# Kernel optimization log

Measured on AMD Instinct MI355X. Metric: run time of the kernel, lower is better.

## Reference

```python
import jax, jax.numpy as jnp
import numpy as np

QB = 127.0  # 2**(8-1) - 1


def ternary_dequant(w):
    # absmean ternary quantization, then dequantize by scale
    scale = jnp.mean(jnp.abs(w))
    w_t = jnp.clip(jnp.round(w / (scale + 1e-8)), -1.0, 1.0)
    w_t = jnp.where(scale == 0.0, jnp.zeros_like(w), w_t)
    return w_t * scale


def activation_quantize(x):
    # per-row (last-dim) absmax int8 fake-quant
    scale = jnp.max(jnp.abs(x), axis=-1, keepdims=True) / QB
    scale = jnp.maximum(scale, 1e-8)
    return jnp.clip(jnp.round(x / scale), -QB, QB) * scale


def setup_inputs() -> dict:
    key = jax.random.key(0)
    kx, kw = jax.random.split(key)
    x = jax.random.normal(kx, (2, 4096, 4096), dtype=jnp.float32)
    # kaiming_uniform-ish init scale; exact init distribution is irrelevant to the math
    bound = 1.0 / np.sqrt(4096)
    weight = jax.random.uniform(kw, (4096, 4096), dtype=jnp.float32,
                                minval=-bound, maxval=bound)
    return {"x": x, "weight": weight}


def reference(x, weight):
    w_q = ternary_dequant(weight)        # [out, in]
    x_q = activation_quantize(x)         # [b, s, in]
    return jnp.einsum('bsi,oi->bso', x_q, w_q)
```

## Files before the change

### kernel.cpp

```cpp
#include <hip/hip_runtime.h>
#include <stdint.h>
#include <stddef.h>


#define K_DIM 4096
#define M_DIM 8192
#define N_DIM 4096

typedef int v4i __attribute__((ext_vector_type(4)));

__device__ __forceinline__ void async_copy16(void* lds, const void* g) {
  __builtin_amdgcn_global_load_lds(
      (const __attribute__((address_space(1))) unsigned int*)g,
      (__attribute__((address_space(3))) unsigned int*)lds,
      16, 0, 0);
}

__global__ void k_wsum(const float* __restrict__ w, double* __restrict__ partials) {
  const float4* w4 = (const float4*)w;
  int tid = blockIdx.x * 256 + threadIdx.x;
  double s = 0.0;
  for (int i = tid; i < 4194304; i += 262144) {
    float4 v = w4[i];
    s += (double)fabsf(v.x) + (double)fabsf(v.y) +
         (double)fabsf(v.z) + (double)fabsf(v.w);
  }
  for (int off = 32; off > 0; off >>= 1) s += __shfl_down(s, off);
  __shared__ double lsum[4];
  int lane = threadIdx.x & 63, wid = threadIdx.x >> 6;
  if (lane == 0) lsum[wid] = s;
  __syncthreads();
  if (threadIdx.x == 0)
    partials[blockIdx.x] = lsum[0] + lsum[1] + lsum[2] + lsum[3];
}

__global__ void k_wscale(const double* __restrict__ partials, float* __restrict__ wscale) {
  double s = 0.0;
  for (int i = threadIdx.x; i < 1024; i += 256) s += partials[i];
  for (int off = 32; off > 0; off >>= 1) s += __shfl_down(s, off);
  __shared__ double lsum[4];
  int lane = threadIdx.x & 63, wid = threadIdx.x >> 6;
  if (lane == 0) lsum[wid] = s;
  __syncthreads();
  if (threadIdx.x == 0) {
    double tot = lsum[0] + lsum[1] + lsum[2] + lsum[3];
    *wscale = (float)(tot / 16777216.0);
  }
}

__global__ void k_wq(const float* __restrict__ w, const float* __restrict__ wscale,
                     char* __restrict__ qw) {
  float d = *wscale + 1e-8f;
  const float4* w4 = (const float4*)w;
  int* q4 = (int*)qw;
  int tid = blockIdx.x * 256 + threadIdx.x;
  for (int i = tid; i < 4194304; i += 524288) {
    float4 v = w4[i];
    int a = (int)fmaxf(fminf(rintf(v.x / d), 1.f), -1.f);
    int b = (int)fmaxf(fminf(rintf(v.y / d), 1.f), -1.f);
    int c = (int)fmaxf(fminf(rintf(v.z / d), 1.f), -1.f);
    int e = (int)fmaxf(fminf(rintf(v.w / d), 1.f), -1.f);
    q4[i] = (a & 255) | ((b & 255) << 8) | ((c & 255) << 16) | ((e & 255) << 24);
  }
}

__global__ void k_xq(const float* __restrict__ x, char* __restrict__ qx,
                     float* __restrict__ sx) {
  int row = blockIdx.x;
  const float4* xr = (const float4*)(x + (size_t)row * K_DIM);
  float4 v[4];
  float m = 0.f;
#pragma unroll
  for (int c = 0; c < 4; c++) {
    v[c] = xr[threadIdx.x + c * 256];
    m = fmaxf(m, fmaxf(fmaxf(fabsf(v[c].x), fabsf(v[c].y)),
                       fmaxf(fabsf(v[c].z), fabsf(v[c].w))));
  }
  for (int off = 32; off > 0; off >>= 1) m = fmaxf(m, __shfl_down(m, off));
  __shared__ float lm[4];
  __shared__ float bscale;
  int lane = threadIdx.x & 63, wid = threadIdx.x >> 6;
  if (lane == 0) lm[wid] = m;
  __syncthreads();
  if (threadIdx.x == 0) {
    float mm = fmaxf(fmaxf(lm[0], lm[1]), fmaxf(lm[2], lm[3]));
    float sc = fmaxf(mm / 127.0f, 1e-8f);
    bscale = sc;
    sx[row] = sc;
  }
  __syncthreads();
  float sc = bscale;
  int* q4 = (int*)(qx + (size_t)row * K_DIM);
#pragma unroll
  for (int c = 0; c < 4; c++) {
    int a = (int)fmaxf(fminf(rintf(v[c].x / sc), 127.f), -127.f);
    int b = (int)fmaxf(fminf(rintf(v[c].y / sc), 127.f), -127.f);
    int cc = (int)fmaxf(fminf(rintf(v[c].z / sc), 127.f), -127.f);
    int e = (int)fmaxf(fminf(rintf(v[c].w / sc), 127.f), -127.f);
    q4[threadIdx.x + c * 256] = (a & 255) | ((b & 255) << 8) | ((cc & 255) << 16) | ((e & 255) << 24);
  }
}

__global__ __launch_bounds__(512, 2) void k_gemm(const char* __restrict__ qx,
                       const char* __restrict__ qw,
                       const float* __restrict__ sx,
                       const float* __restrict__ wscale,
                       float* __restrict__ out) {
  __shared__ char lds[4][32768];

  const int tid = threadIdx.x;
  const int lane = tid & 63;
  const int wave = tid >> 6;
  const int wr = wave >> 2;
  const int wc = wave & 3;

  const int wg = (blockIdx.x & 7) * 64 + (blockIdx.x >> 3);
  const int bm = wg >> 4;
  const int bn = wg & 15;
  const int rowBase = bm * 256;
  const int colBase = bn * 256;

  const int rl = tid >> 2;
  const int kswz = (((tid & 3) ^ ((rl >> 1) & 3)) << 4);
  const char* gA0 = qx + (size_t)(rowBase + rl) * K_DIM + kswz;
  const char* gA1 = gA0 + (size_t)128 * K_DIM;
  const char* gB0 = qw + (size_t)(colBase + rl) * K_DIM + kswz;
  const char* gB1 = gB0 + (size_t)128 * K_DIM;
  const int dOff = wave << 10;

  const int sR = ((lane & 15) >> 1) & 3;
  const int kro = (((lane >> 4) ^ sR) << 4);
  const int aOff = ((wr << 7) + (lane & 15)) * 64 + kro;
  const int bOff = 16384 + ((wc << 6) + (lane & 15)) * 64 + kro;

  v4i acc[8][4] = {};

  auto STAGE = [&](int t) {
    char* b = &lds[t & 3][0];
    const size_t ko = (size_t)t << 6;
    async_copy16(b + dOff,         gA0 + ko);
    async_copy16(b + 8192 + dOff,  gA1 + ko);
    async_copy16(b + 16384 + dOff, gB0 + ko);
    async_copy16(b + 24576 + dOff, gB1 + ko);
  };

  auto COMPUTE = [&](int t) {
    const char* b = &lds[t & 3][0];
    v4i bf[4];
#pragma unroll
    for (int n = 0; n < 4; ++n)
      bf[n] = *(const v4i*)(b + bOff + n * 1024);
    __builtin_amdgcn_s_setprio(1);
#pragma unroll
    for (int m = 0; m < 8; ++m) {
      v4i af = *(const v4i*)(b + aOff + m * 1024);
#pragma unroll
      for (int n = 0; n < 4; ++n)
        acc[m][n] = __builtin_amdgcn_mfma_i32_16x16x64_i8(af, bf[n], acc[m][n], 0, 0, 0);
    }
    __builtin_amdgcn_s_setprio(0);
  };

  STAGE(0); STAGE(1); STAGE(2);

  for (int t = 0; t < 61; ++t) {
    asm volatile("s_waitcnt vmcnt(8)" ::: "memory");
    __builtin_amdgcn_s_barrier();
    STAGE(t + 3);
    COMPUTE(t);
  }
  asm volatile("s_waitcnt vmcnt(8)" ::: "memory");
  __builtin_amdgcn_s_barrier();
  COMPUTE(61);
  asm volatile("s_waitcnt vmcnt(4)" ::: "memory");
  __builtin_amdgcn_s_barrier();
  COMPUTE(62);
  asm volatile("s_waitcnt vmcnt(0)" ::: "memory");
  __builtin_amdgcn_s_barrier();
  COMPUTE(63);

  const float swv = *wscale;
  const int col0 = colBase + (wc << 6) + (lane & 15);
  const int row0 = rowBase + (wr << 7) + ((lane >> 4) << 2);
#pragma unroll
  for (int m = 0; m < 8; ++m) {
#pragma unroll
    for (int r = 0; r < 4; ++r) {
      const int row = row0 + m * 16 + r;
      const float s = sx[row] * swv;
#pragma unroll
      for (int n = 0; n < 4; ++n)
        out[(size_t)row * N_DIM + col0 + n * 16] = (float)acc[m][n][r] * s;
    }
  }
}

extern "C" void kernel_launch(void* const* d_in, const int* in_sizes, int n_in,
                              void* d_out, int out_size, void* d_ws, size_t ws_size,
                              hipStream_t stream) {
  const float* x = (const float*)d_in[0];
  const float* w = (const float*)d_in[1];
  float* out = (float*)d_out;
  char* ws = (char*)d_ws;

  double* partials = (double*)ws;
  float* wscale    = (float*)(ws + 8192);
  float* sx        = (float*)(ws + 8448);
  char*  qw        = ws + 41472;
  char*  qx        = ws + 41472 + 16777216;

  k_wsum  <<<1024, 256, 0, stream>>>(w, partials);
  k_wscale<<<   1, 256, 0, stream>>>(partials, wscale);
  k_wq    <<<2048, 256, 0, stream>>>(w, wscale, qw);
  k_xq    <<<8192, 256, 0, stream>>>(x, qx, sx);
  k_gemm  <<<32 * 16, 512, 0, stream>>>(qx, qw, sx, wscale, out);
}
```

Measured before the change: 394.6 us.

## Split GEMM k-step into four quadrant phases interleaving loads, MFMA and barriers

Restructures the int8 GEMM main loop so each k-tile runs as four quadrant sub-phases. Each phase loads a 4x2 set of A/B fragments from LDS, issues one of the four async global-to-LDS copies for a future stage, synchronises with barriers, and runs 8 MFMAs. The goal is to interleave LDS reads, global loads and matrix-core work more finely, ping-pong style across waves. The cost is eight extra workgroup barriers per k-step and A fragments re-read from LDS twice, either of which may cut throughput.

```diff
diff --git a/kernel.cpp b/kernel.cpp
--- a/kernel.cpp
+++ b/kernel.cpp
@@ -135,49 +135,84 @@
 
   v4i acc[8][4] = {};
 
-  auto STAGE = [&](int t) {
+  auto STAGE1 = [&](int t, int q) {
     char* b = &lds[t & 3][0];
     const size_t ko = (size_t)t << 6;
-    async_copy16(b + dOff,         gA0 + ko);
-    async_copy16(b + 8192 + dOff,  gA1 + ko);
-    async_copy16(b + 16384 + dOff, gB0 + ko);
-    async_copy16(b + 24576 + dOff, gB1 + ko);
+    if (q == 0)      async_copy16(b + dOff,         gA0 + ko);
+    else if (q == 1) async_copy16(b + 8192 + dOff,  gA1 + ko);
+    else if (q == 2) async_copy16(b + 16384 + dOff, gB0 + ko);
+    else             async_copy16(b + 24576 + dOff, gB1 + ko);
   };
 
-  auto COMPUTE = [&](int t) {
-    const char* b = &lds[t & 3][0];
-    v4i bf[4];
-#pragma unroll
-    for (int n = 0; n < 4; ++n)
-      bf[n] = *(const v4i*)(b + bOff + n * 1024);
-    __builtin_amdgcn_s_setprio(1);
-#pragma unroll
-    for (int m = 0; m < 8; ++m) {
-      v4i af = *(const v4i*)(b + aOff + m * 1024);
-#pragma unroll
-      for (int n = 0; n < 4; ++n)
-        acc[m][n] = __builtin_amdgcn_mfma_i32_16x16x64_i8(af, bf[n], acc[m][n], 0, 0, 0);
-    }
-    __builtin_amdgcn_s_setprio(0);
-  };
-
-  STAGE(0); STAGE(1); STAGE(2);
+#pragma unroll
+  for (int q = 0; q < 4; ++q) STAGE1(0, q);
+#pragma unroll
+  for (int q = 0; q < 4; ++q) STAGE1(1, q);
+#pragma unroll
+  for (int q = 0; q < 4; ++q) STAGE1(2, q);
 
   for (int t = 0; t < 61; ++t) {
     asm volatile("s_waitcnt vmcnt(8)" ::: "memory");
     __builtin_amdgcn_s_barrier();
-    STAGE(t + 3);
-    COMPUTE(t);
-  }
-  asm volatile("s_waitcnt vmcnt(8)" ::: "memory");
-  __builtin_amdgcn_s_barrier();
-  COMPUTE(61);
-  asm volatile("s_waitcnt vmcnt(4)" ::: "memory");
-  __builtin_amdgcn_s_barrier();
-  COMPUTE(62);
-  asm volatile("s_waitcnt vmcnt(0)" ::: "memory");
-  __builtin_amdgcn_s_barrier();
-  COMPUTE(63);
+    const char* b = &lds[t & 3][0];
+#pragma unroll
+    for (int q = 0; q < 4; ++q) {
+      const int mh = q >> 1, nh = q & 1;
+      v4i af[4], bf[2];
+#pragma unroll
+      for (int j = 0; j < 4; ++j)
+        af[j] = *(const v4i*)(b + aOff + (mh * 4 + j) * 1024);
+#pragma unroll
+      for (int i = 0; i < 2; ++i)
+        bf[i] = *(const v4i*)(b + bOff + (nh * 2 + i) * 1024);
+      STAGE1(t + 3, q);
+      asm volatile("" ::: "memory");
+      __builtin_amdgcn_s_barrier();
+      asm volatile("s_waitcnt lgkmcnt(0)" ::: "memory");
+      __builtin_amdgcn_s_setprio(1);
+#pragma unroll
+      for (int j = 0; j < 4; ++j)
+#pragma unroll
+        for (int i = 0; i < 2; ++i)
+          acc[mh * 4 + j][nh * 2 + i] = __builtin_amdgcn_mfma_i32_16x16x64_i8(
+              af[j], bf[i], acc[mh * 4 + j][nh * 2 + i], 0, 0, 0);
+      __builtin_amdgcn_s_setprio(0);
+      __builtin_amdgcn_s_barrier();
+    }
+  }
+
+#pragma unroll
+  for (int e = 0; e < 3; ++e) {
+    const int t = 61 + e;
+    if (e == 0)      asm volatile("s_waitcnt vmcnt(8)" ::: "memory");
+    else if (e == 1) asm volatile("s_waitcnt vmcnt(4)" ::: "memory");
+    else             asm volatile("s_waitcnt vmcnt(0)" ::: "memory");
+    __builtin_amdgcn_s_barrier();
+    const char* b = &lds[t & 3][0];
+#pragma unroll
+    for (int q = 0; q < 4; ++q) {
+      const int mh = q >> 1, nh = q & 1;
+      v4i af[4], bf[2];
+#pragma unroll
+      for (int j = 0; j < 4; ++j)
+        af[j] = *(const v4i*)(b + aOff + (mh * 4 + j) * 1024);
+#pragma unroll
+      for (int i = 0; i < 2; ++i)
+        bf[i] = *(const v4i*)(b + bOff + (nh * 2 + i) * 1024);
+      asm volatile("" ::: "memory");
+      __builtin_amdgcn_s_barrier();
+      asm volatile("s_waitcnt lgkmcnt(0)" ::: "memory");
+      __builtin_amdgcn_s_setprio(1);
+#pragma unroll
+      for (int j = 0; j < 4; ++j)
+#pragma unroll
+        for (int i = 0; i < 2; ++i)
+          acc[mh * 4 + j][nh * 2 + i] = __builtin_amdgcn_mfma_i32_16x16x64_i8(
+              af[j], bf[i], acc[mh * 4 + j][nh * 2 + i], 0, 0, 0);
+      __builtin_amdgcn_s_setprio(0);
+      __builtin_amdgcn_s_barrier();
+    }
+  }
 
   const float swv = *wscale;
   const int col0 = colBase + (wc << 6) + (lane & 15);
```

New measurement: 413.2 us. 1.05x slower.

## Double-buffer LDS fragment reads in registers across k-iterations of int8 GEMM

Applied to the files above, without the earlier changes.

The GEMM main loop now prefetches the next k-tile's B fragments and first half of A fragments from LDS into a second register set while the current tile's MFMAs run, ping-ponging between two register buffers. The loop is unrolled by two with explicit prologue and epilogue, and the global-load wait is tightened so the next tile is resident before it is read. The aim is to hide LDS read latency behind MFMA work. In exchange it raises register pressure under the 512x2 launch bounds, which risks spills or lower occupancy, and it shortens the effective global prefetch distance.

```diff
diff --git a/kernel.cpp b/kernel.cpp
--- a/kernel.cpp
+++ b/kernel.cpp
@@ -144,40 +144,78 @@
     async_copy16(b + 24576 + dOff, gB1 + ko);
   };
 
-  auto COMPUTE = [&](int t) {
-    const char* b = &lds[t & 3][0];
-    v4i bf[4];
-#pragma unroll
-    for (int n = 0; n < 4; ++n)
-      bf[n] = *(const v4i*)(b + bOff + n * 1024);
-    __builtin_amdgcn_s_setprio(1);
-#pragma unroll
-    for (int m = 0; m < 8; ++m) {
-      v4i af = *(const v4i*)(b + aOff + m * 1024);
-#pragma unroll
-      for (int n = 0; n < 4; ++n)
-        acc[m][n] = __builtin_amdgcn_mfma_i32_16x16x64_i8(af, bf[n], acc[m][n], 0, 0, 0);
-    }
-    __builtin_amdgcn_s_setprio(0);
-  };
+  v4i afA[4], bfA[4], afB[4], bfB[4];
+
+#define PRE_READ(T, AF, BF)                                                  \
+  {                                                                          \
+    const char* bx_ = &lds[(T) & 3][0];                                      \
+    _Pragma("unroll") for (int j_ = 0; j_ < 4; ++j_)                         \
+        BF[j_] = *(const v4i*)(bx_ + bOff + j_ * 1024);                      \
+    _Pragma("unroll") for (int j_ = 0; j_ < 4; ++j_)                         \
+        AF[j_] = *(const v4i*)(bx_ + aOff + j_ * 1024);                      \
+  }
+
+#define FULL_ITER(T, CURAF, CURBF, NXTAF, NXTBF, DO_STAGE, VMC)              \
+  {                                                                          \
+    asm volatile("s_waitcnt vmcnt(" #VMC ")" ::: "memory");                  \
+    __builtin_amdgcn_s_barrier();                                            \
+    asm volatile("" ::: "memory");                                           \
+    const char* bc_ = &lds[(T) & 3][0];                                      \
+    v4i afL_[4];                                                             \
+    _Pragma("unroll") for (int j_ = 0; j_ < 4; ++j_)                         \
+        afL_[j_] = *(const v4i*)(bc_ + aOff + (4 + j_) * 1024);              \
+    PRE_READ((T) + 1, NXTAF, NXTBF);                                         \
+    if (DO_STAGE) STAGE((T) + 3);                                            \
+    asm volatile("" ::: "memory");                                           \
+    __builtin_amdgcn_s_setprio(1);                                           \
+    _Pragma("unroll") for (int m_ = 0; m_ < 4; ++m_)                         \
+        _Pragma("unroll") for (int n_ = 0; n_ < 4; ++n_)                     \
+            acc[m_][n_] = __builtin_amdgcn_mfma_i32_16x16x64_i8(             \
+                CURAF[m_], CURBF[n_], acc[m_][n_], 0, 0, 0);                 \
+    _Pragma("unroll") for (int m_ = 0; m_ < 4; ++m_)                         \
+        _Pragma("unroll") for (int n_ = 0; n_ < 4; ++n_)                     \
+            acc[4 + m_][n_] = __builtin_amdgcn_mfma_i32_16x16x64_i8(         \
+                afL_[m_], CURBF[n_], acc[4 + m_][n_], 0, 0, 0);              \
+    __builtin_amdgcn_s_setprio(0);                                           \
+  }
 
   STAGE(0); STAGE(1); STAGE(2);
-
-  for (int t = 0; t < 61; ++t) {
-    asm volatile("s_waitcnt vmcnt(8)" ::: "memory");
-    __builtin_amdgcn_s_barrier();
-    STAGE(t + 3);
-    COMPUTE(t);
-  }
   asm volatile("s_waitcnt vmcnt(8)" ::: "memory");
   __builtin_amdgcn_s_barrier();
-  COMPUTE(61);
-  asm volatile("s_waitcnt vmcnt(4)" ::: "memory");
-  __builtin_amdgcn_s_barrier();
-  COMPUTE(62);
-  asm volatile("s_waitcnt vmcnt(0)" ::: "memory");
-  __builtin_amdgcn_s_barrier();
-  COMPUTE(63);
+  asm volatile("" ::: "memory");
+  PRE_READ(0, afA, bfA);
+
+  for (int tp = 0; tp < 30; ++tp) {
+    const int t = tp * 2;
+    FULL_ITER(t,     afA, bfA, afB, bfB, 1, 4);
+    FULL_ITER(t + 1, afB, bfB, afA, bfA, 1, 4);
+  }
+  FULL_ITER(60, afA, bfA, afB, bfB, 1, 4);
+  FULL_ITER(61, afB, bfB, afA, bfA, 0, 4);
+  FULL_ITER(62, afA, bfA, afB, bfB, 0, 0);
+  {
+    const char* bc_ = &lds[63 & 3][0];
+    v4i afL_[4];
+#pragma unroll
+    for (int j_ = 0; j_ < 4; ++j_)
+      afL_[j_] = *(const v4i*)(bc_ + aOff + (4 + j_) * 1024);
+    __builtin_amdgcn_s_setprio(1);
+#pragma unroll
+    for (int m_ = 0; m_ < 4; ++m_)
+#pragma unroll
+      for (int n_ = 0; n_ < 4; ++n_)
+        acc[m_][n_] = __builtin_amdgcn_mfma_i32_16x16x64_i8(
+            afB[m_], bfB[n_], acc[m_][n_], 0, 0, 0);
+#pragma unroll
+    for (int m_ = 0; m_ < 4; ++m_)
+#pragma unroll
+      for (int n_ = 0; n_ < 4; ++n_)
+        acc[4 + m_][n_] = __builtin_amdgcn_mfma_i32_16x16x64_i8(
+            afL_[m_], bfB[n_], acc[4 + m_][n_], 0, 0, 0);
+    __builtin_amdgcn_s_setprio(0);
+  }
+#undef FULL_ITER
+#undef PRE_READ
 
   const float swv = *wscale;
   const int col0 = colBase + (wc << 6) + (lane & 15);
```

New measurement: 389.0 us. Within noise of the previous version (-1.4%).
